# Kernel optimization log

Hardware: AMD Instinct MI355X
Metric: run time of the kernel (lower is better)

The kernel has to match this reference:

```python
import jax, jax.numpy as jnp
import numpy as np

N, E, R, D = 50000, 800000, 12, 64


def setup_inputs() -> dict:
    key = jax.random.key(0)
    ks = jax.random.split(key, 32)
    s = 0.1
    inp = {
        'x': jnp.ones((N, 1), jnp.float32),
        'src': jax.random.randint(ks[0], (E,), 0, N, dtype=jnp.int32),
        'dst': jax.random.randint(ks[1], (E,), 0, N, dtype=jnp.int32),
        'etype': jax.random.randint(ks[2], (E,), 0, R, dtype=jnp.int32),
        'W_emb': s * jax.random.normal(ks[3], (1, D), jnp.float32),
        'b_emb': jnp.zeros((D,), jnp.float32),
    }
    i = 4
    for l in (1, 2, 3):
        inp[f'Wrel{l}'] = s * jax.random.normal(ks[i], (R, D, D), jnp.float32); i += 1
        inp[f'Wself{l}'] = s * jax.random.normal(ks[i], (D, D), jnp.float32); i += 1
        inp[f'b{l}'] = jnp.zeros((D,), jnp.float32)
        inp[f'gatew{l}'] = s * jax.random.normal(ks[i], (D,), jnp.float32); i += 1
        inp[f'gateb{l}'] = jnp.zeros((), jnp.float32)
        inp[f'attn{l}'] = s * jax.random.normal(ks[i], (D,), jnp.float32); i += 1
    inp['Wskip2'] = s * jax.random.normal(ks[i], (D, D), jnp.float32); i += 1
    inp['Wskip3'] = s * jax.random.normal(ks[i], (D, D), jnp.float32)
    return inp


def _segment_softmax(score, seg, n):
    m = jax.ops.segment_max(score, seg, num_segments=n)
    e = jnp.exp(score - m[seg])
    z = jax.ops.segment_sum(e, seg, num_segments=n)
    return e / (z[seg] + 1e-16)


def _rgcn_layer(h, src, dst, etype, Wrel, Wself, b, gw, gb, av, skip_h=None, Wskip=None, act=True):
    n = h.shape[0]
    # transform nodes under every relation, then gather per-edge: avoids [E,din,dout] weight gather
    msgs_all = jnp.einsum('nd,rde->nre', h, Wrel)          # [N,R,dout]
    m = msgs_all[src, etype]                               # [E,dout]
    gate = jax.nn.sigmoid(m @ gw + gb)                     # [E] edge gate
    score = jax.nn.leaky_relu(m @ av)                      # [E] attention logit
    alpha = _segment_softmax(score, dst, n)                # softmax over incoming edges
    m = m * (gate * alpha)[:, None]
    out = jax.ops.segment_sum(m, dst, num_segments=n) + h @ Wself + b
    if skip_h is not None:
        out = out + skip_h @ Wskip
    return jax.nn.relu(out) if act else out


def reference(x, src, dst, etype, W_emb, b_emb,
              Wrel1, Wself1, b1, gatew1, gateb1, attn1,
              Wrel2, Wself2, b2, gatew2, gateb2, attn2,
              Wrel3, Wself3, b3, gatew3, gateb3, attn3,
              Wskip2, Wskip3):
    h0 = jax.nn.relu(x @ W_emb + b_emb)                    # embed layer, [N,D]
    h1 = _rgcn_layer(h0, src, dst, etype, Wrel1, Wself1, b1, gatew1, gateb1, attn1, act=True)
    h2 = _rgcn_layer(h1, src, dst, etype, Wrel2, Wself2, b2, gatew2, gateb2, attn2, h1, Wskip2, act=True)
    h3 = _rgcn_layer(h2, src, dst, etype, Wrel3, Wself3, b3, gatew3, gateb3, attn3, h2, Wskip3, act=False)
    return h3
```

## Files before the change

kernel.cpp:

```cpp
#include <hip/hip_runtime.h>

#define DD 64
#define RR 12
#define KTOT 832
#define NKS 26
#define ASTR 840
#define TROWS 16
#define EPB2 8192

typedef _Float16 half8v __attribute__((ext_vector_type(8)));
typedef __attribute__((ext_vector_type(4))) float f32x4;

__global__ void k_sgw2(const float* __restrict__ x, const float* __restrict__ Wemb,
                       const float* __restrict__ bemb,
                       const float* __restrict__ q, const float* __restrict__ g,
                       const float* __restrict__ gb, float2* __restrict__ EW, int N) {
    __shared__ float We[DD], Be[DD], qs[RR * 65], gs[RR * 65];
    int tid = threadIdx.x;
    if (tid < DD) { We[tid] = Wemb[tid]; Be[tid] = bemb[tid]; }
    for (int i = tid; i < RR * DD; i += 256) {
        int r = i >> 6, c = i & 63;
        qs[r * 65 + c] = q[i];
        gs[r * 65 + c] = g[i];
    }
    __syncthreads();
    int t = blockIdx.x * 256 + tid;
    if (t >= N * RR) return;
    int n = t / RR, r = t - n * RR;
    float xv = x[n];
    const float* qp = qs + r * 65;
    const float* gp = gs + r * 65;
    float aq = 0.f, ag = 0.f;
#pragma unroll
    for (int d = 0; d < DD; d++) {
        float h = fmaf(xv, We[d], Be[d]);
        h = h > 0.f ? h : 0.f;
        aq = fmaf(h, qp[d], aq);
        ag = fmaf(h, gp[d], ag);
    }
    float sc = aq > 0.f ? aq : 0.01f * aq;
    float ev = expf(sc);
    float gate = 1.f / (1.f + expf(-(ag + gb[0])));
    EW[t] = make_float2(ev, ev * gate);
}


__global__ void k_bh(const int* __restrict__ dst, int* __restrict__ bcnt,
                     int E, int nbuck) {
    __shared__ int lh[512];
    int tid = threadIdx.x;
    for (int i = tid; i < 512; i += 512) lh[i] = 0;
    __syncthreads();
    int base = blockIdx.x * EPB2;
    int lim = base + EPB2 < E ? base + EPB2 : E;
    for (int i = base + tid; i < lim; i += 512)
        atomicAdd(&lh[dst[i] >> 7], 1);
    __syncthreads();
    for (int i = tid; i < nbuck; i += 512)
        if (lh[i]) atomicAdd(&bcnt[i], lh[i]);
}

__global__ void k_bscan(const int* __restrict__ bcnt, int* __restrict__ bbase,
                        int* __restrict__ bcur, int nbuck, int E) {
    __shared__ int wsum[8];
    int tid = threadIdx.x, lane = tid & 63, wv = tid >> 6;
    int v = (tid < nbuck) ? bcnt[tid] : 0;
    int incl = v;
#pragma unroll
    for (int d = 1; d < 64; d <<= 1) {
        int t2 = __shfl_up(incl, d);
        if (lane >= d) incl += t2;
    }
    if (lane == 63) wsum[wv] = incl;
    __syncthreads();
    int pre = 0;
#pragma unroll
    for (int w = 0; w < 8; w++) if (w < wv) pre += wsum[w];
    int excl = pre + incl - v;
    if (tid < nbuck) { bbase[tid] = excl; bcur[tid] = excl; }
    if (tid == nbuck - 1) bbase[nbuck] = excl + v;
}

__global__ void k_bscat(const int* __restrict__ src, const int* __restrict__ dst,
                        const int* __restrict__ et, int* __restrict__ bcur,
                        unsigned* __restrict__ epk2, int E, int nbuck) {
    __shared__ int lh[512];
    __shared__ int lcur[512];
    int tid = threadIdx.x;
    for (int i = tid; i < 512; i += 512) lh[i] = 0;
    __syncthreads();
    int base = blockIdx.x * EPB2;
    int lim = base + EPB2 < E ? base + EPB2 : E;
    for (int i = base + tid; i < lim; i += 512)
        atomicAdd(&lh[dst[i] >> 7], 1);
    __syncthreads();
    for (int i = tid; i < nbuck; i += 512)
        lcur[i] = lh[i] ? atomicAdd(&bcur[i], lh[i]) : 0;
    __syncthreads();
    for (int i = base + tid; i < lim; i += 512) {
        int d = dst[i];
        int pos = atomicAdd(&lcur[d >> 7], 1);
        epk2[pos] = ((unsigned)(d & 127) << 20) | ((unsigned)et[i] << 16) | (unsigned)src[i];
    }
}

__global__ void k_b2(const unsigned* __restrict__ epk2, const int* __restrict__ bbase,
                     unsigned* __restrict__ epk, int* __restrict__ offd,
                     int N, int E) {
    int b = blockIdx.x, tid = threadIdx.x;
    int p0 = bbase[b], p1 = bbase[b + 1], cb = p1 - p0;
    __shared__ int hist[128], cur[128];
    __shared__ unsigned stg[4096];
    if (tid < 128) hist[tid] = 0;
    __syncthreads();
    for (int i = tid; i < cb; i += 256)
        atomicAdd(&hist[(epk2[p0 + i] >> 20) & 127], 1);
    __syncthreads();
    if (tid == 0) {
        int a = 0;
        for (int j = 0; j < 128; j++) { int c = hist[j]; hist[j] = a; a += c; }
    }
    __syncthreads();
    if (tid < 128) {
        cur[tid] = hist[tid];
        int node = b * 128 + tid;
        if (node < N) offd[node] = p0 + hist[tid];
    }
    if (b == 0 && tid == 0) offd[N] = E;
    __syncthreads();
    if (cb <= 4096) {
        for (int i = tid; i < cb; i += 256) {
            unsigned pk = epk2[p0 + i];
            int pos = atomicAdd(&cur[(pk >> 20) & 127], 1);
            stg[pos] = pk & 0xFFFFFu;
        }
        __syncthreads();
        for (int i = tid; i < cb; i += 256) epk[p0 + i] = stg[i];
    } else {
        for (int i = tid; i < cb; i += 256) {
            unsigned pk = epk2[p0 + i];
            int pos = atomicAdd(&cur[(pk >> 20) & 127], 1);
            epk[p0 + pos] = pk & 0xFFFFFu;
        }
    }
}

__global__ void k_wprep3(
    const float* __restrict__ Wr0, const float* __restrict__ Ws0, const float* __restrict__ Wk0,
    const float* __restrict__ av0, const float* __restrict__ gw0,
    _Float16* __restrict__ Bh0, _Float16* __restrict__ Bl0, float* __restrict__ q0, float* __restrict__ g0,
    const float* __restrict__ Wr1, const float* __restrict__ Ws1, const float* __restrict__ Wk1,
    const float* __restrict__ av1, const float* __restrict__ gw1,
    _Float16* __restrict__ Bh1, _Float16* __restrict__ Bl1, float* __restrict__ q1, float* __restrict__ g1,
    const float* __restrict__ Wr2, const float* __restrict__ Ws2, const float* __restrict__ Wk2,
    const float* __restrict__ av2, const float* __restrict__ gw2,
    _Float16* __restrict__ Bh2, _Float16* __restrict__ Bl2, float* __restrict__ q2, float* __restrict__ g2) {
    int layer = blockIdx.x / (NKS + 3);
    int bx = blockIdx.x % (NKS + 3);
    const float* Wrel  = layer == 0 ? Wr0 : layer == 1 ? Wr1 : Wr2;
    const float* Wself = layer == 0 ? Ws0 : layer == 1 ? Ws1 : Ws2;
    const float* Wskip = layer == 0 ? Wk0 : layer == 1 ? Wk1 : Wk2;
    const float* av    = layer == 0 ? av0 : layer == 1 ? av1 : av2;
    const float* gw    = layer == 0 ? gw0 : layer == 1 ? gw1 : gw2;
    _Float16* Bh = layer == 0 ? Bh0 : layer == 1 ? Bh1 : Bh2;
    _Float16* Bl = layer == 0 ? Bl0 : layer == 1 ? Bl1 : Bl2;
    float* q = layer == 0 ? q0 : layer == 1 ? q1 : q2;
    float* g = layer == 0 ? g0 : layer == 1 ? g1 : g2;

    if (bx < NKS) {
        int t = bx * 256 + threadIdx.x;
        int ks = t >> 8, ct = (t >> 6) & 3, lane = t & 63;
        int col = ct * 16 + (lane & 15);
        int kb = ks * 32 + ((lane >> 4) << 3);
        _Float16* ph = Bh + (size_t)t * 8;
        _Float16* pl = Bl + (size_t)t * 8;
#pragma unroll
        for (int i = 0; i < 8; i++) {
            int k = kb + i;
            float v;
            if (k < 768) v = Wrel[(size_t)k * DD + col];
            else {
                v = Wself[(size_t)(k - 768) * DD + col];
                if (Wskip) v += Wskip[(size_t)(k - 768) * DD + col];
            }
            _Float16 h = (_Float16)v;
            ph[i] = h;
            pl[i] = (_Float16)(v - (float)h);
        }
    } else {
        int t = (bx - NKS) * 256 + threadIdx.x;
        if (t >= RR * DD) return;
        const float* wp = Wrel + (size_t)t * DD;
        float aq = 0.f, ag = 0.f;
#pragma unroll
        for (int e = 0; e < DD; e++) { float w = wp[e]; aq += w * av[e]; ag += w * gw[e]; }
        q[t] = aq; g[t] = ag;
    }
}

#define AGG_EDGE(ee, wy, hh)                                       \
    switch (ee) {                                                  \
        case 0:  acc[0]  = fmaf(wy, hh, acc[0]);  break;           \
        case 1:  acc[1]  = fmaf(wy, hh, acc[1]);  break;           \
        case 2:  acc[2]  = fmaf(wy, hh, acc[2]);  break;           \
        case 3:  acc[3]  = fmaf(wy, hh, acc[3]);  break;           \
        case 4:  acc[4]  = fmaf(wy, hh, acc[4]);  break;           \
        case 5:  acc[5]  = fmaf(wy, hh, acc[5]);  break;           \
        case 6:  acc[6]  = fmaf(wy, hh, acc[6]);  break;           \
        case 7:  acc[7]  = fmaf(wy, hh, acc[7]);  break;           \
        case 8:  acc[8]  = fmaf(wy, hh, acc[8]);  break;           \
        case 9:  acc[9]  = fmaf(wy, hh, acc[9]);  break;           \
        case 10: acc[10] = fmaf(wy, hh, acc[10]); break;           \
        default: acc[11] = fmaf(wy, hh, acc[11]); break;           \
    }

template<int NB, bool MASKED, int XD>
__device__ __forceinline__ void ebatch(const unsigned* __restrict__ epk,
                                       const float2* __restrict__ EWr,
                                       const _Float16* __restrict__ hin16,
                                       const float* __restrict__ xsrc,
                                       float we_r, float be_r,
                                       int p, int p1, int lane,
                                       float acc[RR], float& zacc) {
    int len = p1 - p;
    unsigned pk[NB];
    float2 ew[NB];
#pragma unroll
    for (int i = 0; i < NB; i++) {
        int ii = MASKED ? (i < len ? i : len - 1) : i;
        pk[i] = epk[p + ii];
    }
#pragma unroll
    for (int i = 0; i < NB; i++)
        ew[i] = EWr[(size_t)(pk[i] & 0xFFFFu) * RR + ((pk[i] >> 16) & 15u)];
    if (XD) {
        float xs[NB];
#pragma unroll
        for (int i = 0; i < NB; i++) xs[i] = xsrc[pk[i] & 0xFFFFu];
        __builtin_amdgcn_sched_barrier(0);
#pragma unroll
        for (int i = 0; i < NB; i++) {
            int e = __builtin_amdgcn_readfirstlane((int)((pk[i] >> 16) & 15u));
            float hh = fmaf(xs[i], we_r, be_r);
            hh = hh > 0.f ? hh : 0.f;
            float wx = ew[i].x, wy = ew[i].y;
            if (MASKED && i >= 1) {
                bool ok = i < len;
                wx = ok ? wx : 0.f;
                wy = ok ? wy : 0.f;
            }
            zacc += wx;
            AGG_EDGE(e, wy, hh);
        }
    } else {
        _Float16 hr[NB];
#pragma unroll
        for (int i = 0; i < NB; i++)
            hr[i] = hin16[(size_t)(pk[i] & 0xFFFFu) * DD + lane];
        __builtin_amdgcn_sched_barrier(0);
#pragma unroll
        for (int i = 0; i < NB; i++) {
            int e = __builtin_amdgcn_readfirstlane((int)((pk[i] >> 16) & 15u));
            float hh = (float)hr[i];
            float wx = ew[i].x, wy = ew[i].y;
            if (MASKED && i >= 1) {
                bool ok = i < len;
                wx = ok ? wx : 0.f;
                wy = ok ? wy : 0.f;
            }
            zacc += wx;
            AGG_EDGE(e, wy, hh);
        }
    }
}

template<int XD>
__global__ void __launch_bounds__(512, 8)
k_fused(const unsigned* __restrict__ epk, const int* __restrict__ offd,
        const _Float16* __restrict__ hin16,
        const float* __restrict__ xsrc, const float* __restrict__ Wemb,
        const float* __restrict__ bemb,
        const float2* __restrict__ EWr, float2* __restrict__ EWw,
        const _Float16* __restrict__ Bh, const _Float16* __restrict__ Bl,
        const float* __restrict__ bias, float* __restrict__ out,
        _Float16* __restrict__ hout16, int N, int act,
        const float* __restrict__ qn, const float* __restrict__ gn,
        const float* __restrict__ gbn) {
    __shared__ __align__(16) _Float16 At[TROWS * ASTR];
    __shared__ __align__(16) float Hf[TROWS * 68];
    __shared__ __align__(16) float qg[2 * RR * 68];
    __shared__ int offs[TROWS + 1];
    __shared__ int claim;
    int tid = threadIdx.x, lane = tid & 63, w = tid >> 6;
    int nb0 = blockIdx.x * TROWS;
    if (tid == 0) claim = 0;
    if (tid < TROWS + 1) {
        int nn = nb0 + tid;
        offs[tid] = (nn <= N) ? offd[nn] : 0;
    }
    if (EWw) {
        for (int i = tid; i < RR * DD; i += 512) {
            int r = i >> 6, c = i & 63;
            qg[r * 68 + c] = qn[i];
            qg[816 + r * 68 + c] = gn[i];
        }
    }
    float we_r = 0.f, be_r = 0.f;
    if (XD) { we_r = Wemb[lane]; be_r = bemb[lane]; }
    __syncthreads();

    for (;;) {
        int t0 = 0;
        if (lane == 0) t0 = atomicAdd(&claim, 1);
        int nl = __builtin_amdgcn_readfirstlane(t0);
        if (nl >= TROWS) break;
        int node = nb0 + nl;
        _Float16* Ar = At + nl * ASTR;
        if (node >= N) {
            for (int k = lane; k < KTOT; k += 64) Ar[k] = (_Float16)0.f;
            continue;
        }
        int p0 = __builtin_amdgcn_readfirstlane(offs[nl]);
        int p1 = __builtin_amdgcn_readfirstlane(offs[nl + 1]);

        float acc[RR];
#pragma unroll
        for (int r = 0; r < RR; r++) acc[r] = 0.f;
        float zacc = 0.f;
        int p = p0;
        while (p + 16 <= p1) {
            ebatch<16, false, XD>(epk, EWr, hin16, xsrc, we_r, be_r, p, p1, lane, acc, zacc);
            p += 16;
        }
        int rem = p1 - p;
        if (rem > 8)      ebatch<16, true, XD>(epk, EWr, hin16, xsrc, we_r, be_r, p, p1, lane, acc, zacc);
        else if (rem > 0) ebatch<8, true, XD>(epk, EWr, hin16, xsrc, we_r, be_r, p, p1, lane, acc, zacc);

        float inv = 1.f / (zacc + 1e-16f);
#pragma unroll
        for (int r = 0; r < RR; r++) Ar[r * DD + lane] = (_Float16)(acc[r] * inv);
        if (XD) {
            float h0v = fmaf(xsrc[node], we_r, be_r);
            h0v = h0v > 0.f ? h0v : 0.f;
            Ar[768 + lane] = (_Float16)h0v;
        } else {
            Ar[768 + lane] = hin16[(size_t)node * DD + lane];
        }
    }
    __syncthreads();

    if (w < 4) {
        const half8v* Bh8 = (const half8v*)Bh;
        const half8v* Bl8 = (const half8v*)Bl;
        const _Float16* abase = At + (lane & 15) * ASTR + ((lane >> 4) << 3);
        f32x4 acc0 = {0.f, 0.f, 0.f, 0.f};
#pragma unroll 4
        for (int ks = 0; ks < NKS; ++ks) {
            half8v ah = *(const half8v*)(abase + ks * 32);
            size_t bb = (size_t)(ks * 4 + w) * 64 + lane;
            half8v bh = Bh8[bb];
            half8v bl = Bl8[bb];
            acc0 = __builtin_amdgcn_mfma_f32_16x16x32_f16(ah, bh, acc0, 0, 0, 0);
            acc0 = __builtin_amdgcn_mfma_f32_16x16x32_f16(ah, bl, acc0, 0, 0, 0);
        }

        int colb = lane & 15, kg = lane >> 4;
        int c = w * 16 + colb;
        float bv = bias[c];
#pragma unroll
        for (int j = 0; j < 4; j++) {
            int rl = kg * 4 + j;
            int row = nb0 + rl;
            if (row < N) {
                float v = acc0[j] + bv;
                if (act) v = v > 0.f ? v : 0.f;
                if (out) out[(size_t)row * DD + c] = v;
                if (hout16) hout16[(size_t)row * DD + c] = (_Float16)v;
                if (EWw) Hf[rl * 68 + c] = v;
            }
        }
    }

    if (EWw) {
        __syncthreads();
        if (tid < TROWS * RR) {
            int nl = tid / RR, r = tid - nl * RR;
            int node = nb0 + nl;
            if (node < N) {
                const float* hp = Hf + nl * 68;
                const float* qp = qg + r * 68;
                const float* gp = qg + 816 + r * 68;
                float aq = 0.f, ag = 0.f;
#pragma unroll
                for (int c4 = 0; c4 < 16; c4++) {
                    float4 hv = *(const float4*)(hp + c4 * 4);
                    float4 qv = *(const float4*)(qp + c4 * 4);
                    float4 gv = *(const float4*)(gp + c4 * 4);
                    aq += hv.x * qv.x + hv.y * qv.y + hv.z * qv.z + hv.w * qv.w;
                    ag += hv.x * gv.x + hv.y * gv.y + hv.z * gv.z + hv.w * gv.w;
                }
                float sc = aq > 0.f ? aq : 0.01f * aq;
                float ev = expf(sc);
                float gate = 1.f / (1.f + expf(-(ag + gbn[0])));
                EWw[(size_t)node * RR + r] = make_float2(ev, ev * gate);
            }
        }
    }
}

extern "C" void kernel_launch(void* const* d_in, const int* in_sizes, int n_in,
                              void* d_out, int out_size, void* d_ws, size_t ws_size,
                              hipStream_t stream) {
    const float* x    = (const float*)d_in[0];
    const int*   src  = (const int*)d_in[1];
    const int*   dst  = (const int*)d_in[2];
    const int*   etyp = (const int*)d_in[3];
    const float* Wemb = (const float*)d_in[4];
    const float* bemb = (const float*)d_in[5];
    const int N = in_sizes[0];
    const int E = in_sizes[1];
    const int nbuck = (N + 127) >> 7;
    const int nblk2 = (E + EPB2 - 1) / EPB2;

    const float* Wrel[3];  const float* Wself[3]; const float* bb[3];
    const float* gwv[3];   const float* gbv[3];   const float* av[3];
    for (int l = 0; l < 3; l++) {
        int o = 6 + 6 * l;
        Wrel[l]  = (const float*)d_in[o + 0];
        Wself[l] = (const float*)d_in[o + 1];
        bb[l]    = (const float*)d_in[o + 2];
        gwv[l]   = (const float*)d_in[o + 3];
        gbv[l]   = (const float*)d_in[o + 4];
        av[l]    = (const float*)d_in[o + 5];
    }
    const float* Wskip[3] = { nullptr, (const float*)d_in[24], (const float*)d_in[25] };

    float* p = (float*)d_ws;
    _Float16* h16A = (_Float16*)p; p += (size_t)N * DD / 2;
    _Float16* h16B = (_Float16*)p; p += (size_t)N * DD / 2;
    float2* EWa = (float2*)p; p += (size_t)N * RR * 2;
    float2* EWb = (float2*)p; p += (size_t)N * RR * 2;
    float* qv3[3]; float* gv3[3]; _Float16* Bh3[3]; _Float16* Bl3[3];
    for (int l = 0; l < 3; l++) {
        qv3[l] = p; p += RR * DD;
        gv3[l] = p; p += RR * DD;
        Bh3[l] = (_Float16*)p; p += NKS * 4 * 64 * 8 / 2;
        Bl3[l] = (_Float16*)p; p += NKS * 4 * 64 * 8 / 2;
    }
    unsigned* epk2 = (unsigned*)p; p += E;
    unsigned* epk  = (unsigned*)p; p += E;
    int* bcnt  = (int*)p; p += 512;
    int* bbase = (int*)p; p += 516;
    int* bcur  = (int*)p; p += 512;
    int* offd  = (int*)p; p += N + 4;

    const int B = 256;

    k_wprep3<<<3 * (NKS + 3), B, 0, stream>>>(
        Wrel[0], Wself[0], Wskip[0], av[0], gwv[0], Bh3[0], Bl3[0], qv3[0], gv3[0],
        Wrel[1], Wself[1], Wskip[1], av[1], gwv[1], Bh3[1], Bl3[1], qv3[1], gv3[1],
        Wrel[2], Wself[2], Wskip[2], av[2], gwv[2], Bh3[2], Bl3[2], qv3[2], gv3[2]);

    hipMemsetAsync(bcnt, 0, 512 * 4, stream);
    k_bh<<<nblk2, 512, 0, stream>>>(dst, bcnt, E, nbuck);
    k_bscan<<<1, 512, 0, stream>>>(bcnt, bbase, bcur, nbuck, E);
    k_bscat<<<nblk2, 512, 0, stream>>>(src, dst, etyp, bcur, epk2, E, nbuck);
    k_b2<<<nbuck, 256, 0, stream>>>(epk2, bbase, epk, offd, N, E);

    k_sgw2<<<(N * RR + B - 1) / B, B, 0, stream>>>(x, Wemb, bemb, qv3[0], gv3[0],
                                                   gbv[0], EWa, N);

    const int fblocks = (N + TROWS - 1) / TROWS;

    k_fused<1><<<fblocks, 512, 0, stream>>>(epk, offd, nullptr, x, Wemb, bemb,
                                            EWa, EWb, Bh3[0], Bl3[0], bb[0],
                                            nullptr, h16B, N, 1,
                                            qv3[1], gv3[1], gbv[1]);
    k_fused<0><<<fblocks, 512, 0, stream>>>(epk, offd, h16B, nullptr, nullptr, nullptr,
                                            EWb, EWa, Bh3[1], Bl3[1], bb[1],
                                            nullptr, h16A, N, 1,
                                            qv3[2], gv3[2], gbv[2]);
    k_fused<0><<<fblocks, 512, 0, stream>>>(epk, offd, h16A, nullptr, nullptr, nullptr,
                                            EWa, nullptr, Bh3[2], Bl3[2], bb[2],
                                            (float*)d_out, nullptr, N, 0,
                                            nullptr, nullptr, nullptr);
}
```

Before: 220.8 us.

## Sort edges by (dst, etype) so aggregation uses a running accumulator

The bucket sort in k_b2 now keys each edge on destination node and relation type, so edges within a node's segment are grouped by relation. The aggregation loop then keeps a single running register accumulator and only writes it into the per-relation array when the relation changes, replacing a 12-way switch executed per edge. This adds a larger shared histogram, a per-node prefix scan, and a wave-level scan in the sort kernel. Masked tail edges still take the flush branch. Flushing assigns rather than adds, which depends on each relation appearing as one contiguous run.

```diff
diff --git a/kernel.cpp b/kernel.cpp
--- a/kernel.cpp
+++ b/kernel.cpp
@@ -109,29 +109,54 @@
                      int N, int E) {
     int b = blockIdx.x, tid = threadIdx.x;
     int p0 = bbase[b], p1 = bbase[b + 1], cb = p1 - p0;
-    __shared__ int hist[128], cur[128];
+    __shared__ int hist[1536];
+    __shared__ int cur[1536];
+    __shared__ int nodeTot[128], nodeExcl[128];
+    __shared__ int wsum1;
     __shared__ unsigned stg[4096];
-    if (tid < 128) hist[tid] = 0;
-    __syncthreads();
-    for (int i = tid; i < cb; i += 256)
-        atomicAdd(&hist[(epk2[p0 + i] >> 20) & 127], 1);
-    __syncthreads();
-    if (tid == 0) {
-        int a = 0;
-        for (int j = 0; j < 128; j++) { int c = hist[j]; hist[j] = a; a += c; }
-    }
-    __syncthreads();
+    for (int i = tid; i < 1536; i += 256) hist[i] = 0;
+    __syncthreads();
+    for (int i = tid; i < cb; i += 256) {
+        unsigned pk = epk2[p0 + i];
+        int key = (int)((pk >> 20) & 127u) * 12 + (int)((pk >> 16) & 15u);
+        atomicAdd(&hist[key], 1);
+    }
+    __syncthreads();
+    int incl = 0, v = 0;
     if (tid < 128) {
-        cur[tid] = hist[tid];
+        int base = tid * 12, s = 0;
+#pragma unroll
+        for (int j = 0; j < 12; j++) { int c = hist[base + j]; hist[base + j] = s; s += c; }
+        nodeTot[tid] = s;
+        v = s; incl = s;
+        int lane = tid & 63;
+#pragma unroll
+        for (int d = 1; d < 64; d <<= 1) {
+            int t2 = __shfl_up(incl, d);
+            if (lane >= d) incl += t2;
+        }
+        if (tid == 63) wsum1 = incl;
+    }
+    __syncthreads();
+    if (tid < 128) {
+        int pre = (tid >= 64) ? wsum1 : 0;
+        nodeExcl[tid] = pre + incl - v;
+    }
+    __syncthreads();
+    if (tid < 128) {
         int node = b * 128 + tid;
-        if (node < N) offd[node] = p0 + hist[tid];
+        int base = tid * 12;
+        if (node < N) offd[node] = p0 + nodeExcl[tid];
+#pragma unroll
+        for (int j = 0; j < 12; j++) cur[base + j] = nodeExcl[tid] + hist[base + j];
     }
     if (b == 0 && tid == 0) offd[N] = E;
     __syncthreads();
     if (cb <= 4096) {
         for (int i = tid; i < cb; i += 256) {
             unsigned pk = epk2[p0 + i];
-            int pos = atomicAdd(&cur[(pk >> 20) & 127], 1);
+            int key = (int)((pk >> 20) & 127u) * 12 + (int)((pk >> 16) & 15u);
+            int pos = atomicAdd(&cur[key], 1);
             stg[pos] = pk & 0xFFFFFu;
         }
         __syncthreads();
@@ -139,7 +164,8 @@
     } else {
         for (int i = tid; i < cb; i += 256) {
             unsigned pk = epk2[p0 + i];
-            int pos = atomicAdd(&cur[(pk >> 20) & 127], 1);
+            int key = (int)((pk >> 20) & 127u) * 12 + (int)((pk >> 16) & 15u);
+            int pos = atomicAdd(&cur[key], 1);
             epk[p0 + pos] = pk & 0xFFFFFu;
         }
     }
@@ -198,20 +224,20 @@
     }
 }
 
-#define AGG_EDGE(ee, wy, hh)                                       \
-    switch (ee) {                                                  \
-        case 0:  acc[0]  = fmaf(wy, hh, acc[0]);  break;           \
-        case 1:  acc[1]  = fmaf(wy, hh, acc[1]);  break;           \
-        case 2:  acc[2]  = fmaf(wy, hh, acc[2]);  break;           \
-        case 3:  acc[3]  = fmaf(wy, hh, acc[3]);  break;           \
-        case 4:  acc[4]  = fmaf(wy, hh, acc[4]);  break;           \
-        case 5:  acc[5]  = fmaf(wy, hh, acc[5]);  break;           \
-        case 6:  acc[6]  = fmaf(wy, hh, acc[6]);  break;           \
-        case 7:  acc[7]  = fmaf(wy, hh, acc[7]);  break;           \
-        case 8:  acc[8]  = fmaf(wy, hh, acc[8]);  break;           \
-        case 9:  acc[9]  = fmaf(wy, hh, acc[9]);  break;           \
-        case 10: acc[10] = fmaf(wy, hh, acc[10]); break;           \
-        default: acc[11] = fmaf(wy, hh, acc[11]); break;           \
+#define FLUSH_RACC()                                               \
+    switch (cur_e) {                                               \
+        case 0:  acc[0]  = racc; break;                            \
+        case 1:  acc[1]  = racc; break;                            \
+        case 2:  acc[2]  = racc; break;                            \
+        case 3:  acc[3]  = racc; break;                            \
+        case 4:  acc[4]  = racc; break;                            \
+        case 5:  acc[5]  = racc; break;                            \
+        case 6:  acc[6]  = racc; break;                            \
+        case 7:  acc[7]  = racc; break;                            \
+        case 8:  acc[8]  = racc; break;                            \
+        case 9:  acc[9]  = racc; break;                            \
+        case 10: acc[10] = racc; break;                            \
+        default: acc[11] = racc; break;                            \
     }
 
 template<int NB, bool MASKED, int XD>
@@ -221,7 +247,8 @@
                                        const float* __restrict__ xsrc,
                                        float we_r, float be_r,
                                        int p, int p1, int lane,
-                                       float acc[RR], float& zacc) {
+                                       float acc[RR], float& zacc,
+                                       int& cur_e, float& racc) {
     int len = p1 - p;
     unsigned pk[NB];
     float2 ew[NB];
@@ -241,6 +268,7 @@
 #pragma unroll
         for (int i = 0; i < NB; i++) {
             int e = __builtin_amdgcn_readfirstlane((int)((pk[i] >> 16) & 15u));
+            if (e != cur_e) { FLUSH_RACC(); racc = 0.f; cur_e = e; }
             float hh = fmaf(xs[i], we_r, be_r);
             hh = hh > 0.f ? hh : 0.f;
             float wx = ew[i].x, wy = ew[i].y;
@@ -250,7 +278,7 @@
                 wy = ok ? wy : 0.f;
             }
             zacc += wx;
-            AGG_EDGE(e, wy, hh);
+            racc = fmaf(wy, hh, racc);
         }
     } else {
         _Float16 hr[NB];
@@ -261,6 +289,7 @@
 #pragma unroll
         for (int i = 0; i < NB; i++) {
             int e = __builtin_amdgcn_readfirstlane((int)((pk[i] >> 16) & 15u));
+            if (e != cur_e) { FLUSH_RACC(); racc = 0.f; cur_e = e; }
             float hh = (float)hr[i];
             float wx = ew[i].x, wy = ew[i].y;
             if (MASKED && i >= 1) {
@@ -269,7 +298,7 @@
                 wy = ok ? wy : 0.f;
             }
             zacc += wx;
-            AGG_EDGE(e, wy, hh);
+            racc = fmaf(wy, hh, racc);
         }
     }
 }
@@ -327,14 +356,20 @@
 #pragma unroll
         for (int r = 0; r < RR; r++) acc[r] = 0.f;
         float zacc = 0.f;
+        float racc = 0.f;
+        int cur_e = (p0 < p1) ? (int)((epk[p0] >> 16) & 15u) : 0;
         int p = p0;
         while (p + 16 <= p1) {
-            ebatch<16, false, XD>(epk, EWr, hin16, xsrc, we_r, be_r, p, p1, lane, acc, zacc);
+            ebatch<16, false, XD>(epk, EWr, hin16, xsrc, we_r, be_r, p, p1, lane,
+                                  acc, zacc, cur_e, racc);
             p += 16;
         }
         int rem = p1 - p;
-        if (rem > 8)      ebatch<16, true, XD>(epk, EWr, hin16, xsrc, we_r, be_r, p, p1, lane, acc, zacc);
-        else if (rem > 0) ebatch<8, true, XD>(epk, EWr, hin16, xsrc, we_r, be_r, p, p1, lane, acc, zacc);
+        if (rem > 8)      ebatch<16, true, XD>(epk, EWr, hin16, xsrc, we_r, be_r, p, p1, lane,
+                                               acc, zacc, cur_e, racc);
+        else if (rem > 0) ebatch<8, true, XD>(epk, EWr, hin16, xsrc, we_r, be_r, p, p1, lane,
+                                              acc, zacc, cur_e, racc);
+        FLUSH_RACC();
 
         float inv = 1.f / (zacc + 1e-16f);
 #pragma unroll
```

Measured after the change: 243.6 us. 10.3% more time.
